# Optimization experiments

Hardware: AMD Instinct MI355X
Metric: run time of the kernel (lower is better)

The kernel has to match this reference:

```python
import jax, jax.numpy as jnp
import numpy as np

N_NODES = 100000
N_EDGES = 1600000
N_GRAPHS = 256
D_IN = 128
D_HID = 128
D_OUT = 64


def graph_conv(x, src, dst, W_rel, b_rel, W_root):
    # PyG GraphConv: out = lin_rel(mean_{j->i} x_j) + lin_root(x)
    msgs = jax.ops.segment_sum(x[src], dst, num_segments=N_NODES)  # [N, d]
    deg = jax.ops.segment_sum(jnp.ones((src.shape[0],), x.dtype), dst, num_segments=N_NODES)
    agg = msgs / jnp.maximum(deg, 1.0)[:, None]
    return agg @ W_rel + b_rel + x @ W_root


def setup_inputs() -> dict:
    key = jax.random.key(0)
    ks = jax.random.split(key, 12)
    x = jax.random.normal(ks[0], (N_NODES, D_IN), dtype=jnp.float32)
    edge_index = jax.random.randint(ks[1], (2, N_EDGES), 0, N_NODES, dtype=jnp.int64)
    batch = jnp.sort(jax.random.randint(ks[2], (N_NODES,), 0, N_GRAPHS, dtype=jnp.int64))
    def lin(k, fan_in, fan_out):
        bound = 1.0 / np.sqrt(fan_in)
        return jax.random.uniform(k, (fan_in, fan_out), jnp.float32, -bound, bound)
    inp = {
        "x": x, "edge_index": edge_index, "batch": batch,
        "W1_rel": lin(ks[3], D_IN, D_HID), "b1_rel": jnp.zeros((D_HID,), jnp.float32), "W1_root": lin(ks[4], D_IN, D_HID),
        "W2_rel": lin(ks[5], D_HID, D_HID), "b2_rel": jnp.zeros((D_HID,), jnp.float32), "W2_root": lin(ks[6], D_HID, D_HID),
        "W3_rel": lin(ks[7], D_HID, D_HID), "b3_rel": jnp.zeros((D_HID,), jnp.float32), "W3_root": lin(ks[8], D_HID, D_HID),
        "Wl": lin(ks[9], D_HID, D_OUT), "bl": jnp.zeros((D_OUT,), jnp.float32),
    }
    return inp


def reference(x, edge_index, batch, W1_rel, b1_rel, W1_root, W2_rel, b2_rel, W2_root,
              W3_rel, b3_rel, W3_root, Wl, bl):
    src, dst = edge_index[0], edge_index[1]
    h = jax.nn.relu(graph_conv(x, src, dst, W1_rel, b1_rel, W1_root))
    h = jax.nn.relu(graph_conv(h, src, dst, W2_rel, b2_rel, W2_root))
    h = graph_conv(h, src, dst, W3_rel, b3_rel, W3_root)
    # global mean pool over graphs
    sums = jax.ops.segment_sum(h, batch, num_segments=N_GRAPHS)          # [G, d]
    cnts = jax.ops.segment_sum(jnp.ones((h.shape[0],), h.dtype), batch, num_segments=N_GRAPHS)
    pooled = sums / jnp.maximum(cnts, 1.0)[:, None]
    # dropout is identity at inference
    return pooled @ Wl + bl  # [G, D_OUT]
```

## Files before the change

### kernel.cpp

```cpp
#include <hip/hip_runtime.h>
#include <hip/hip_bf16.h>

#define N_NODES  100000
#define N_EDGES  1600000
#define N_GRAPHS 256
#define DCH      128
#define DOUT     64
#define NB       391
#define PADB     512
#define SLACK    4608
#define CHUNK    4096
#define PCH      64

typedef short v8s __attribute__((ext_vector_type(8)));
typedef float v4f __attribute__((ext_vector_type(4)));

static __device__ __forceinline__ float bf2f(unsigned short u) {
    unsigned int x = ((unsigned int)u) << 16;
    return __builtin_bit_cast(float, x);
}
static __device__ __forceinline__ unsigned short f2bf(float f) {
    unsigned int x = __builtin_bit_cast(unsigned int, f);
    unsigned int r = (x + 0x7fffu + ((x >> 16) & 1u)) >> 16;
    return (unsigned short)r;
}
static __device__ __forceinline__ int clampi(int v, int lo, int hi) {
    return v < lo ? lo : (v > hi ? hi : v);
}

__global__ void cvt_kernel(const float* __restrict__ in, unsigned short* __restrict__ out) {
    size_t i = ((size_t)blockIdx.x * blockDim.x + threadIdx.x) * 4;
    if (i + 3 < (size_t)N_NODES * DCH) {
        float4 f = *reinterpret_cast<const float4*>(in + i);
        uint2 o;
        o.x = ((unsigned)f2bf(f.y) << 16) | (unsigned)f2bf(f.x);
        o.y = ((unsigned)f2bf(f.w) << 16) | (unsigned)f2bf(f.z);
        *reinterpret_cast<uint2*>(out + i) = o;
    }
}

__global__ void __launch_bounds__(256) binA_kernel(const int* __restrict__ src, const int* __restrict__ dst,
                                                   int* __restrict__ gcur, uint2* __restrict__ region) {
    __shared__ uint2 stage[CHUNK];
    __shared__ int hcnt[PADB], hcnt2[PADB], hoff[PADB], garr[PADB];
    __shared__ int s2[256];
    int tid = threadIdx.x;
    int e0  = blockIdx.x * CHUNK;
    int nedge = N_EDGES - e0; if (nedge > CHUNK) nedge = CHUNK;

    for (int b = tid; b < PADB; b += 256) { hcnt[b] = 0; hcnt2[b] = 0; }
    __syncthreads();

    int es[16], ed[16];
    #pragma unroll
    for (int j = 0; j < 16; j++) {
        int e = e0 + j * 256 + tid;
        if (e < N_EDGES) {
            es[j] = clampi(src[e], 0, N_NODES - 1);
            ed[j] = clampi(dst[e], 0, N_NODES - 1);
            atomicAdd(&hcnt[ed[j] >> 8], 1);
        } else { es[j] = -1; ed[j] = 0; }
    }
    __syncthreads();

    int v0 = hcnt[2 * tid], v1 = hcnt[2 * tid + 1];
    s2[tid] = v0 + v1; __syncthreads();
    for (int off = 1; off < 256; off <<= 1) {
        int x = (tid >= off) ? s2[tid - off] : 0;
        __syncthreads();
        s2[tid] += x;
        __syncthreads();
    }
    int excl = s2[tid] - (v0 + v1);
    hoff[2 * tid] = excl; hoff[2 * tid + 1] = excl + v0;
    __syncthreads();

    for (int b = tid; b < NB; b += 256) {
        int c = hcnt[b];
        garr[b] = b * SLACK + ((c > 0) ? atomicAdd(&gcur[b], c) : 0);
    }
    __syncthreads();

    #pragma unroll
    for (int j = 0; j < 16; j++) {
        if (es[j] >= 0) {
            int b = ed[j] >> 8;
            int pos = atomicAdd(&hcnt2[b], 1) + hoff[b];
            stage[pos] = (uint2){(unsigned)es[j], (unsigned)ed[j]};
        }
    }
    __syncthreads();

    for (int i = tid; i < nedge; i += 256) {
        uint2 en = stage[i];
        int b = (int)(en.y >> 8);
        int gpos = garr[b] + (i - hoff[b]);
        if (gpos < (b + 1) * SLACK) region[gpos] = en;
    }
}

__global__ void bucketScan_kernel(const int* __restrict__ gcur, int* __restrict__ rowptrBase,
                                  int* __restrict__ rowptr) {
    __shared__ int s[512];
    int t = threadIdx.x;
    int c = 0;
    if (t < NB) { c = gcur[t]; if (c > SLACK) c = SLACK; }
    s[t] = c; __syncthreads();
    for (int off = 1; off < 512; off <<= 1) {
        int x = (t >= off) ? s[t - off] : 0;
        __syncthreads();
        s[t] += x;
        __syncthreads();
    }
    rowptrBase[t] = s[t] - c;
    if (t == 511) rowptr[N_NODES] = s[511];
}

__global__ void __launch_bounds__(256) binCount_kernel(const uint2* __restrict__ region, const int* __restrict__ gcur,
                                                       const int* __restrict__ rowptrBase, int* __restrict__ rowptr) {
    __shared__ int h[256];
    __shared__ int sc[256];
    int b = blockIdx.x, tid = threadIdx.x;
    h[tid] = 0; __syncthreads();
    int size = gcur[b]; if (size > SLACK) size = SLACK;
    int node0 = b * 256;
    for (int j = tid; j < size; j += 256) {
        unsigned loc = region[b * SLACK + j].y - (unsigned)node0;
        if (loc < 256u) atomicAdd(&h[loc], 1);
    }
    __syncthreads();
    int v = h[tid]; sc[tid] = v; __syncthreads();
    for (int off = 1; off < 256; off <<= 1) {
        int x = (tid >= off) ? sc[tid - off] : 0;
        __syncthreads();
        sc[tid] += x;
        __syncthreads();
    }
    int node = node0 + tid;
    if (node < N_NODES) rowptr[node] = rowptrBase[b] + sc[tid] - v;
}

__global__ void __launch_bounds__(256) binB_kernel(const uint2* __restrict__ region, const int* __restrict__ gcur,
                                                   const int* __restrict__ rowptr, int* __restrict__ csr) {
    __shared__ int cur[256];
    int b   = blockIdx.x;
    int tid = threadIdx.x;
    int node0 = b * 256;
    int nmax  = N_NODES - node0; if (nmax > 256) nmax = 256;
    if (tid < nmax) cur[tid] = rowptr[node0 + tid];
    __syncthreads();
    int size = gcur[b]; if (size > SLACK) size = SLACK;
    for (int j = tid; j < size; j += 256) {
        uint2 en = region[b * SLACK + j];
        unsigned loc = en.y - (unsigned)node0;
        if (loc < 256u) {
            int p = atomicAdd(&cur[loc], 1);
            if (p >= 0 && p < N_EDGES) csr[p] = (int)en.x;
        }
    }
}

__global__ void wfrag_kernel(const float* __restrict__ W1rel, const float* __restrict__ W1root,
                             const float* __restrict__ W2rel, const float* __restrict__ W2root,
                             const float* __restrict__ W3rel, const float* __restrict__ W3root,
                             unsigned short* __restrict__ frag) {
    int gid = blockIdx.x * blockDim.x + threadIdx.x;
    if (gid >= 3 * 8 * 8 * 64) return;
    int lane = gid & 63;
    int nt   = (gid >> 6) & 7;
    int kt   = (gid >> 9) & 7;
    int L    = gid >> 12;
    const float* rel  = (L == 0) ? W1rel  : (L == 1) ? W2rel  : W3rel;
    const float* root = (L == 0) ? W1root : (L == 1) ? W2root : W3root;
    int n  = nt * 16 + (lane & 15);
    int k0 = kt * 32 + (lane >> 4) * 8;
    unsigned short o[8];
    #pragma unroll
    for (int j = 0; j < 8; j++) {
        int k = k0 + j;
        float w = (k < 128) ? rel[k * 128 + n] : root[(k - 128) * 128 + n];
        o[j] = f2bf(w);
    }
    uint4 u;
    u.x = (unsigned)o[0] | ((unsigned)o[1] << 16);
    u.y = (unsigned)o[2] | ((unsigned)o[3] << 16);
    u.z = (unsigned)o[4] | ((unsigned)o[5] << 16);
    u.w = (unsigned)o[6] | ((unsigned)o[7] << 16);
    *reinterpret_cast<uint4*>(frag + (size_t)gid * 8) = u;
}

__global__ void agg_kernel(const unsigned short* __restrict__ hin, const int* __restrict__ rowptr,
                           const int* __restrict__ csr, unsigned short* __restrict__ agg) {
    int wave = threadIdx.x >> 6;
    int lane = threadIdx.x & 63;
    int node = blockIdx.x * 4 + wave;
    if (node >= N_NODES) return;
    int r0 = rowptr[node], r1 = rowptr[node + 1];
    int l16 = lane & 15;
    float a0 = 0.f, a1 = 0.f;
    for (int c = r0; c < r1; c += 16) {
        int m = r1 - c; if (m > 16) m = 16;
        int idx = csr[c + (l16 < m ? l16 : 0)];
        #pragma unroll
        for (int j = 0; j < 16; j++) {
            int s = __shfl(idx, j);
            unsigned int v = *reinterpret_cast<const unsigned int*>(hin + (size_t)s * DCH + lane * 2);
            float w = (j < m) ? 1.0f : 0.0f;
            a0 = fmaf(w, bf2f((unsigned short)(v & 0xffffu)), a0);
            a1 = fmaf(w, bf2f((unsigned short)(v >> 16)), a1);
        }
    }
    int deg = r1 - r0;
    float inv = 1.0f / (float)(deg > 1 ? deg : 1);
    a0 *= inv; a1 *= inv;
    unsigned int o = ((unsigned int)f2bf(a1) << 16) | (unsigned int)f2bf(a0);
    *reinterpret_cast<unsigned int*>(agg + (size_t)node * DCH + lane * 2) = o;
}

__global__ void gemm_kernel(const unsigned short* agg, const unsigned short* __restrict__ root,
                            const unsigned short* __restrict__ frag, const float* __restrict__ bias,
                            unsigned short* hout, int relu) {
    int wave = threadIdx.x >> 6;
    int lane = threadIdx.x & 63;
    int quad = lane >> 4;
    int ml   = lane & 15;
    int base = blockIdx.x * 128 + wave * 32;
    int r0 = clampi(base + ml, 0, N_NODES - 1);
    int r1 = clampi(base + 16 + ml, 0, N_NODES - 1);
    v4f acc[2][8];
    #pragma unroll
    for (int h = 0; h < 2; h++)
        #pragma unroll
        for (int nt = 0; nt < 8; nt++) acc[h][nt] = (v4f){0.f, 0.f, 0.f, 0.f};
    #pragma unroll
    for (int kt = 0; kt < 8; kt++) {
        const unsigned short* asrc = (kt < 4) ? agg : root;
        int ak = (kt & 3) * 32 + quad * 8;
        v8s a0 = *reinterpret_cast<const v8s*>(asrc + (size_t)r0 * DCH + ak);
        v8s a1 = *reinterpret_cast<const v8s*>(asrc + (size_t)r1 * DCH + ak);
        #pragma unroll
        for (int nt = 0; nt < 8; nt++) {
            v8s b = *reinterpret_cast<const v8s*>(frag + (((size_t)(kt * 8 + nt)) * 64 + lane) * 8);
            acc[0][nt] = __builtin_amdgcn_mfma_f32_16x16x32_bf16(a0, b, acc[0][nt], 0, 0, 0);
            acc[1][nt] = __builtin_amdgcn_mfma_f32_16x16x32_bf16(a1, b, acc[1][nt], 0, 0, 0);
        }
    }
    #pragma unroll
    for (int h = 0; h < 2; h++) {
        int mbase = base + h * 16 + quad * 4;
        #pragma unroll
        for (int nt = 0; nt < 8; nt++) {
            int n = nt * 16 + ml;
            float bv = bias[n];
            #pragma unroll
            for (int r = 0; r < 4; r++) {
                int row = mbase + r;
                if (row < N_NODES) {
                    float v = acc[h][nt][r] + bv;
                    if (relu) v = fmaxf(v, 0.f);
                    hout[(size_t)row * DCH + n] = f2bf(v);
                }
            }
        }
    }
}

__global__ void __launch_bounds__(128) pool_kernel(const unsigned short* __restrict__ h,
                                                   const int* __restrict__ batch,
                                                   float* __restrict__ psum) {
    int c  = threadIdx.x;
    int n0 = blockIdx.x * PCH;
    int n1 = n0 + PCH < N_NODES ? n0 + PCH : N_NODES;
    if (n0 >= n1) return;
    int cur = clampi(batch[n0], 0, N_GRAPHS - 1);
    float acc = 0.f;
    for (int n = n0; n < n1; n++) {
        int g = clampi(batch[n], 0, N_GRAPHS - 1);
        if (g != cur) {
            atomicAdd(&psum[cur * DCH + c], acc);
            acc = 0.f; cur = g;
        }
        acc += bf2f(h[(size_t)n * DCH + c]);
    }
    atomicAdd(&psum[cur * DCH + c], acc);
}

static __device__ __forceinline__ int lowerb(const int* __restrict__ a, int n, int key) {
    int lo = 0, hi = n;
    while (lo < hi) { int mid = (lo + hi) >> 1; if (a[mid] < key) lo = mid + 1; else hi = mid; }
    return lo;
}

__global__ void __launch_bounds__(64) final_kernel(const float* __restrict__ psum,
                                                   const int* __restrict__ batch,
                                                   const float* __restrict__ Wl, const float* __restrict__ bl,
                                                   float* __restrict__ out) {
    __shared__ float ps[DCH];
    __shared__ int bounds[2];
    int g = blockIdx.x, tid = threadIdx.x;
    if (tid == 0) {
        bounds[0] = lowerb(batch, N_NODES, g);
        bounds[1] = lowerb(batch, N_NODES, g + 1);
    }
    __syncthreads();
    int cnt = bounds[1] - bounds[0];
    float inv = 1.0f / (float)(cnt > 1 ? cnt : 1);
    ps[tid] = psum[g * DCH + tid] * inv;
    ps[tid + 64] = psum[g * DCH + tid + 64] * inv;
    __syncthreads();
    float o = 0.f;
    #pragma unroll 4
    for (int c = 0; c < DCH; c++) o += ps[c] * Wl[c * DOUT + tid];
    out[g * DOUT + tid] = o + bl[tid];
}

extern "C" void kernel_launch(void* const* d_in, const int* in_sizes, int n_in,
                              void* d_out, int out_size, void* d_ws, size_t ws_size,
                              hipStream_t stream) {
    const float* x     = (const float*)d_in[0];
    const int*   edge  = (const int*)d_in[1];
    const int*   src   = edge;
    const int*   dst   = edge + N_EDGES;
    const int*   batch = (const int*)d_in[2];
    const float* W1rel  = (const float*)d_in[3];
    const float* b1     = (const float*)d_in[4];
    const float* W1root = (const float*)d_in[5];
    const float* W2rel  = (const float*)d_in[6];
    const float* b2     = (const float*)d_in[7];
    const float* W2root = (const float*)d_in[8];
    const float* W3rel  = (const float*)d_in[9];
    const float* b3     = (const float*)d_in[10];
    const float* W3root = (const float*)d_in[11];
    const float* Wl     = (const float*)d_in[12];
    const float* bl     = (const float*)d_in[13];
    float* out = (float*)d_out;

    char* ws = (char*)d_ws;
    size_t off = 0;
    auto carve = [&](size_t bytes) -> void* {
        void* p = ws + off;
        off += (bytes + 255) & ~(size_t)255;
        return p;
    };
    int*            rowptr  = (int*)carve((size_t)(N_NODES + 1) * 4);
    int*            csr     = (int*)carve((size_t)N_EDGES * 4);
    int*            gcur    = (int*)carve((size_t)PADB * 4);
    int*            rpbase  = (int*)carve((size_t)(PADB + 1) * 4);
    unsigned short* frag    = (unsigned short*)carve((size_t)3 * 8 * 8 * 64 * 8 * 2);
    unsigned short* B1      = (unsigned short*)carve((size_t)N_NODES * DCH * 2);
    unsigned short* B2      = (unsigned short*)carve((size_t)N_NODES * DCH * 2);
    float*          psum    = (float*)carve((size_t)N_GRAPHS * DCH * 4);
    uint2*          region  = (uint2*)B1;

    hipMemsetAsync(gcur, 0, (size_t)PADB * 4, stream);
    hipMemsetAsync(psum, 0, (size_t)N_GRAPHS * DCH * 4, stream);

    binA_kernel<<<(N_EDGES + CHUNK - 1) / CHUNK, 256, 0, stream>>>(src, dst, gcur, region);
    bucketScan_kernel<<<1, 512, 0, stream>>>(gcur, rpbase, rowptr);
    binCount_kernel<<<NB, 256, 0, stream>>>(region, gcur, rpbase, rowptr);
    binB_kernel<<<NB, 256, 0, stream>>>(region, gcur, rowptr, csr);
    cvt_kernel<<<(N_NODES * DCH / 4 + 255) / 256, 256, 0, stream>>>(x, B2);
    wfrag_kernel<<<(3 * 8 * 8 * 64 + 255) / 256, 256, 0, stream>>>(W1rel, W1root, W2rel, W2root, W3rel, W3root, frag);

    const int aggGrid  = (N_NODES + 3) / 4;
    const int gemmGrid = (N_NODES + 127) / 128;

    agg_kernel<<<aggGrid, 256, 0, stream>>>(B2, rowptr, csr, B1);
    gemm_kernel<<<gemmGrid, 256, 0, stream>>>(B1, B2, frag, b1, B1, 1);
    agg_kernel<<<aggGrid, 256, 0, stream>>>(B1, rowptr, csr, B2);
    gemm_kernel<<<gemmGrid, 256, 0, stream>>>(B2, B1, frag + 32768, b2, B2, 1);
    agg_kernel<<<aggGrid, 256, 0, stream>>>(B2, rowptr, csr, B1);
    gemm_kernel<<<gemmGrid, 256, 0, stream>>>(B1, B2, frag + 65536, b3, B1, 0);

    pool_kernel<<<(N_NODES + PCH - 1) / PCH, 128, 0, stream>>>(B1, batch, psum);
    final_kernel<<<N_GRAPHS, 64, 0, stream>>>(psum, batch, Wl, bl, out);
}
```

Measured before the change: 454.3 us.

## Fuse CSR build kernels, halve binning chunk, stage GEMM weights in LDS

Merges the bucket scan, per-node count and CSR scatter kernels into one binFinish kernel in which every block redundantly scans the bucket counts, and merges the two memsets into one. It halves the edge chunk per binning block to get more blocks and less register use. It also copies the 64KB weight fragment set into LDS in the GEMM kernel and sets launch bounds to two blocks per SM. These cut launch count and global weight reads, but add redundant scan work and an LDS preload per GEMM block, and the 64KB LDS may limit occupancy.

```diff
diff --git a/kernel.cpp b/kernel.cpp
--- a/kernel.cpp
+++ b/kernel.cpp
@@ -9,7 +9,7 @@
 #define NB       391
 #define PADB     512
 #define SLACK    4608
-#define CHUNK    4096
+#define CHUNK    2048
 #define PCH      64
 
 typedef short v8s __attribute__((ext_vector_type(8)));
@@ -51,9 +51,9 @@
     for (int b = tid; b < PADB; b += 256) { hcnt[b] = 0; hcnt2[b] = 0; }
     __syncthreads();
 
-    int es[16], ed[16];
-    #pragma unroll
-    for (int j = 0; j < 16; j++) {
+    int es[8], ed[8];
+    #pragma unroll
+    for (int j = 0; j < 8; j++) {
         int e = e0 + j * 256 + tid;
         if (e < N_EDGES) {
             es[j] = clampi(src[e], 0, N_NODES - 1);
@@ -82,7 +82,7 @@
     __syncthreads();
 
     #pragma unroll
-    for (int j = 0; j < 16; j++) {
+    for (int j = 0; j < 8; j++) {
         if (es[j] >= 0) {
             int b = ed[j] >> 8;
             int pos = atomicAdd(&hcnt2[b], 1) + hoff[b];
@@ -99,29 +99,26 @@
     }
 }
 
-__global__ void bucketScan_kernel(const int* __restrict__ gcur, int* __restrict__ rowptrBase,
-                                  int* __restrict__ rowptr) {
-    __shared__ int s[512];
-    int t = threadIdx.x;
-    int c = 0;
-    if (t < NB) { c = gcur[t]; if (c > SLACK) c = SLACK; }
-    s[t] = c; __syncthreads();
-    for (int off = 1; off < 512; off <<= 1) {
-        int x = (t >= off) ? s[t - off] : 0;
-        __syncthreads();
-        s[t] += x;
-        __syncthreads();
-    }
-    rowptrBase[t] = s[t] - c;
-    if (t == 511) rowptr[N_NODES] = s[511];
-}
-
-__global__ void __launch_bounds__(256) binCount_kernel(const uint2* __restrict__ region, const int* __restrict__ gcur,
-                                                       const int* __restrict__ rowptrBase, int* __restrict__ rowptr) {
-    __shared__ int h[256];
-    __shared__ int sc[256];
+__global__ void __launch_bounds__(256) binFinish_kernel(const uint2* __restrict__ region, const int* __restrict__ gcur,
+                                                        int* __restrict__ rowptr, int* __restrict__ csr) {
+    __shared__ int h[256], sc[256], cur[256], s2[256], hoff[PADB];
     int b = blockIdx.x, tid = threadIdx.x;
-    h[tid] = 0; __syncthreads();
+    int c0 = gcur[2 * tid];     if (c0 > SLACK) c0 = SLACK;
+    int c1 = gcur[2 * tid + 1]; if (c1 > SLACK) c1 = SLACK;
+    s2[tid] = c0 + c1;
+    h[tid] = 0;
+    __syncthreads();
+    for (int off = 1; off < 256; off <<= 1) {
+        int x = (tid >= off) ? s2[tid - off] : 0;
+        __syncthreads();
+        s2[tid] += x;
+        __syncthreads();
+    }
+    int excl = s2[tid] - (c0 + c1);
+    hoff[2 * tid] = excl; hoff[2 * tid + 1] = excl + c0;
+    __syncthreads();
+    if (b == 0 && tid == 255) rowptr[N_NODES] = hoff[511];
+    int base = hoff[b];
     int size = gcur[b]; if (size > SLACK) size = SLACK;
     int node0 = b * 256;
     for (int j = tid; j < size; j += 256) {
@@ -136,20 +133,11 @@
         sc[tid] += x;
         __syncthreads();
     }
+    int myptr = base + sc[tid] - v;
     int node = node0 + tid;
-    if (node < N_NODES) rowptr[node] = rowptrBase[b] + sc[tid] - v;
-}
-
-__global__ void __launch_bounds__(256) binB_kernel(const uint2* __restrict__ region, const int* __restrict__ gcur,
-                                                   const int* __restrict__ rowptr, int* __restrict__ csr) {
-    __shared__ int cur[256];
-    int b   = blockIdx.x;
-    int tid = threadIdx.x;
-    int node0 = b * 256;
-    int nmax  = N_NODES - node0; if (nmax > 256) nmax = 256;
-    if (tid < nmax) cur[tid] = rowptr[node0 + tid];
-    __syncthreads();
-    int size = gcur[b]; if (size > SLACK) size = SLACK;
+    if (node < N_NODES) rowptr[node] = myptr;
+    cur[tid] = myptr;
+    __syncthreads();
     for (int j = tid; j < size; j += 256) {
         uint2 en = region[b * SLACK + j];
         unsigned loc = en.y - (unsigned)node0;
@@ -217,9 +205,15 @@
     *reinterpret_cast<unsigned int*>(agg + (size_t)node * DCH + lane * 2) = o;
 }
 
-__global__ void gemm_kernel(const unsigned short* agg, const unsigned short* __restrict__ root,
-                            const unsigned short* __restrict__ frag, const float* __restrict__ bias,
-                            unsigned short* hout, int relu) {
+__global__ void __launch_bounds__(256, 2) gemm_kernel(const unsigned short* agg, const unsigned short* __restrict__ root,
+                                                      const unsigned short* __restrict__ frag, const float* __restrict__ bias,
+                                                      unsigned short* hout, int relu) {
+    __shared__ uint4 sB[4096];
+    for (int i = threadIdx.x; i < 4096; i += 256)
+        sB[i] = reinterpret_cast<const uint4*>(frag)[i];
+    __syncthreads();
+    const unsigned short* sBs = reinterpret_cast<const unsigned short*>(sB);
+
     int wave = threadIdx.x >> 6;
     int lane = threadIdx.x & 63;
     int quad = lane >> 4;
@@ -240,7 +234,7 @@
         v8s a1 = *reinterpret_cast<const v8s*>(asrc + (size_t)r1 * DCH + ak);
         #pragma unroll
         for (int nt = 0; nt < 8; nt++) {
-            v8s b = *reinterpret_cast<const v8s*>(frag + (((size_t)(kt * 8 + nt)) * 64 + lane) * 8);
+            v8s b = *reinterpret_cast<const v8s*>(sBs + (((size_t)(kt * 8 + nt)) * 64 + lane) * 8);
             acc[0][nt] = __builtin_amdgcn_mfma_f32_16x16x32_bf16(a0, b, acc[0][nt], 0, 0, 0);
             acc[1][nt] = __builtin_amdgcn_mfma_f32_16x16x32_bf16(a1, b, acc[1][nt], 0, 0, 0);
         }
@@ -344,21 +338,17 @@
     };
     int*            rowptr  = (int*)carve((size_t)(N_NODES + 1) * 4);
     int*            csr     = (int*)carve((size_t)N_EDGES * 4);
-    int*            gcur    = (int*)carve((size_t)PADB * 4);
-    int*            rpbase  = (int*)carve((size_t)(PADB + 1) * 4);
+    int*            gcur    = (int*)carve((size_t)PADB * 4 + (size_t)N_GRAPHS * DCH * 4);
+    float*          psum    = (float*)(gcur + PADB);
     unsigned short* frag    = (unsigned short*)carve((size_t)3 * 8 * 8 * 64 * 8 * 2);
     unsigned short* B1      = (unsigned short*)carve((size_t)N_NODES * DCH * 2);
     unsigned short* B2      = (unsigned short*)carve((size_t)N_NODES * DCH * 2);
-    float*          psum    = (float*)carve((size_t)N_GRAPHS * DCH * 4);
     uint2*          region  = (uint2*)B1;
 
-    hipMemsetAsync(gcur, 0, (size_t)PADB * 4, stream);
-    hipMemsetAsync(psum, 0, (size_t)N_GRAPHS * DCH * 4, stream);
+    hipMemsetAsync(gcur, 0, (size_t)PADB * 4 + (size_t)N_GRAPHS * DCH * 4, stream);
 
     binA_kernel<<<(N_EDGES + CHUNK - 1) / CHUNK, 256, 0, stream>>>(src, dst, gcur, region);
-    bucketScan_kernel<<<1, 512, 0, stream>>>(gcur, rpbase, rowptr);
-    binCount_kernel<<<NB, 256, 0, stream>>>(region, gcur, rpbase, rowptr);
-    binB_kernel<<<NB, 256, 0, stream>>>(region, gcur, rowptr, csr);
+    binFinish_kernel<<<NB, 256, 0, stream>>>(region, gcur, rowptr, csr);
     cvt_kernel<<<(N_NODES * DCH / 4 + 255) / 256, 256, 0, stream>>>(x, B2);
     wfrag_kernel<<<(3 * 8 * 8 * 64 + 255) / 256, 256, 0, stream>>>(W1rel, W1root, W2rel, W2root, W3rel, W3root, frag);
 
```

Measured after the change: 478.7 us. +5.4%, slower.
